# Kernel optimization log

Hardware: AMD Instinct MI355X
Metric: run time of the kernel (lower is better)

The kernel has to match this reference:

```python
import jax, jax.numpy as jnp
import numpy as np

D_MODEL = 512
BINS = 64


def setup_inputs() -> dict:
    key = jax.random.key(0)
    ks = jax.random.split(key, 5)
    x = jax.random.normal(ks[0], (1, 512, D_MODEL), dtype=jnp.float32)
    # torch Linear(2d, d): weight [d, 2d]; store transposed [2d, d] for x @ W
    s1 = 1.0 / np.sqrt(2 * D_MODEL)
    W1 = jax.random.uniform(ks[1], (2 * D_MODEL, D_MODEL), jnp.float32, -s1, s1)
    b1 = jax.random.uniform(ks[2], (D_MODEL,), jnp.float32, -s1, s1)
    s2 = 1.0 / np.sqrt(D_MODEL)
    W2 = jax.random.uniform(ks[3], (D_MODEL, BINS), jnp.float32, -s2, s2)
    b2 = jax.random.uniform(ks[4], (BINS,), jnp.float32, -s2, s2)
    return {"x": x, "W1": W1, "b1": b1, "W2": W2, "b2": b2}


def reference(x, W1, b1, W2, b2):
    # pair = cat([xi, xj], -1); Linear(cat) == xi @ W1[:d] + xj @ W1[d:]
    # This factorization is exact and avoids materializing the [B,N,N,2d] tensor.
    d = x.shape[-1]
    hi = jnp.einsum('bnd,de->bne', x, W1[:d])      # [B, N, d]
    hj = jnp.einsum('bnd,de->bne', x, W1[d:])      # [B, N, d]
    h = hi[:, :, None, :] + hj[:, None, :, :] + b1  # [B, N, N, d]
    h = jax.nn.gelu(h, approximate=False)           # torch nn.GELU default is exact
    return jnp.einsum('bijd,de->bije', h, W2) + b2  # [B, N, N, bins]
```

## Files before the change

kernel.cpp:

```cpp
#include <hip/hip_runtime.h>
#include <hip/hip_fp16.h>

#define D 512
#define NTOK 512
#define BINS 64

typedef float v4f __attribute__((ext_vector_type(4)));
typedef int v4i __attribute__((ext_vector_type(4)));
typedef short short8 __attribute__((ext_vector_type(8)));
typedef _Float16 h8 __attribute__((ext_vector_type(8)));
typedef _Float16 h4 __attribute__((ext_vector_type(4)));

__device__ __forceinline__ __half2 gelu2(__half2 x) {
    __half2 s = __hmul2(x, x);
    __half2 q = __hmul2(x, __hfma2(s, __float2half2_rn(-0.1029437f),
                                      __float2half2_rn(-2.3022082f)));
    __half2 e = h2exp2(q);
    __half2 r = h2rcp(__hadd2(e, __float2half2_rn(1.0f)));
    return __hmul2(x, r);
}

__device__ __forceinline__ __half2 bc_h2(int v) { return __builtin_bit_cast(__half2, v); }
__device__ __forceinline__ int bc_i(__half2 v) { return __builtin_bit_cast(int, v); }

__device__ __forceinline__ v4i pack8(v4f a, v4f b) {
    h8 o;
    o[0] = (_Float16)a.x; o[1] = (_Float16)a.y; o[2] = (_Float16)a.z; o[3] = (_Float16)a.w;
    o[4] = (_Float16)b.x; o[5] = (_Float16)b.y; o[6] = (_Float16)b.z; o[7] = (_Float16)b.w;
    return __builtin_bit_cast(v4i, o);
}

__global__ __launch_bounds__(256) void k_pack(const float* __restrict__ x,
                                              const float* __restrict__ W1,
                                              const float* __restrict__ W2,
                                              v4i* __restrict__ Ap,
                                              v4i* __restrict__ Wp,
                                              short8* __restrict__ Bp) {
    const int b = blockIdx.x;
    const int t = threadIdx.x;
    if (b < 32) {
        const int rb = b;
#pragma unroll
        for (int u = 0; u < 4; ++u) {
            const int e = t + 256 * u;
            const int l = e & 63, ks = e >> 6;
            const float* src = x + (size_t)(rb * 16 + (l & 15)) * D + ks * 32 + (l >> 4) * 8;
            v4f a = *(const v4f*)src;
            v4f c = *(const v4f*)(src + 4);
            Ap[(size_t)(rb * 16 + ks) * 64 + l] = pack8(a, c);
        }
    } else if (b < 96) {
        const int nb = b - 32;
#pragma unroll
        for (int u = 0; u < 4; ++u) {
            const int e = t + 256 * u;
            const int l = e & 63, ks = e >> 6;
            const int ng = nb * 16 + (l & 15);
            const float* src = W1 + (size_t)((ng >> 9) * D + ks * 32 + (l >> 4) * 8) * D
                                  + (ng & 511);
            h8 o;
#pragma unroll
            for (int j = 0; j < 8; ++j) o[j] = (_Float16)src[(size_t)j * D];
            Wp[(size_t)(nb * 16 + ks) * 64 + l] = __builtin_bit_cast(v4i, o);
        }
    } else {
        const int tid = (b - 96) * 256 + t;
        const int ll = tid & 63;
        const int nt = (tid >> 6) & 3;
        const int kt = tid >> 8;
        const int colp = nt * 16 + (ll & 15);
        const int krow = kt * 32 + (ll >> 4) * 8;
        short8 v;
#pragma unroll
        for (int u = 0; u < 8; ++u) {
            _Float16 hv = (_Float16)W2[(size_t)(krow + u) * BINS + colp];
            v[u] = __builtin_bit_cast(short, hv);
        }
        Bp[tid] = v;
    }
}

__global__ __launch_bounds__(256) void k_gemm(const v4i* __restrict__ Ap,
                                              const v4i* __restrict__ Wp,
                                              const float* __restrict__ b1,
                                              _Float16* __restrict__ hi,
                                              _Float16* __restrict__ hj) {
    const int l = threadIdx.x & 63;
    const int w = threadIdx.x >> 6;
    const int c = l & 15;
    const int q = l >> 4;
    const int mb = blockIdx.x >> 4;
    const int cb = blockIdx.x & 15;
    const int nb = cb * 4 + w;

    const v4i* ap0 = Ap + (size_t)(mb * 2 + 0) * 16 * 64 + l;
    const v4i* ap1 = Ap + (size_t)(mb * 2 + 1) * 16 * 64 + l;
    const v4i* wp  = Wp + (size_t)nb * 16 * 64 + l;

    v4f acc0 = {0.f, 0.f, 0.f, 0.f};
    v4f acc1 = {0.f, 0.f, 0.f, 0.f};
#pragma unroll 4
    for (int ks = 0; ks < 16; ++ks) {
        v4i a0 = ap0[ks * 64];
        v4i a1 = ap1[ks * 64];
        v4i bb = wp[ks * 64];
        h8 bf = __builtin_bit_cast(h8, bb);
        acc0 = __builtin_amdgcn_mfma_f32_16x16x32_f16(__builtin_bit_cast(h8, a0), bf, acc0, 0, 0, 0);
        acc1 = __builtin_amdgcn_mfma_f32_16x16x32_f16(__builtin_bit_cast(h8, a1), bf, acc1, 0, 0, 0);
    }

    const int ng = nb * 16 + c;
    const float b1v = (ng < D) ? b1[ng] : 0.0f;
    _Float16* dst = (ng < D ? hi : hj) + (ng & 511);
#pragma unroll
    for (int mf = 0; mf < 2; ++mf) {
        v4f acc = mf ? acc1 : acc0;
        const int row0 = mb * 32 + mf * 16 + q * 4;
#pragma unroll
        for (int r = 0; r < 4; ++r)
            dst[(size_t)(row0 + r) * D] = (_Float16)(acc[r] + b1v);
    }
}

__global__ __launch_bounds__(256) void k_main(const __half* __restrict__ hi,
                                              const __half* __restrict__ hj,
                                              const v4i* __restrict__ Bp,
                                              const float* __restrict__ b2,
                                              float* __restrict__ out) {
    const int l = threadIdx.x & 63;
    const int w = threadIdx.x >> 6;
    const int c = l & 15;
    const int q = l >> 4;
    const int ib = (blockIdx.x >> 5) * 16;
    const int j0 = (blockIdx.x & 31) * 16;

    __shared__ __align__(16) short hic[16][72];
    __shared__ __align__(16) short hjc[16][72];

    const int t = threadIdx.x;
    const int lr = (t & 127) >> 3;
    const int lc = (t & 7) * 8;
    const __half* gsrc = (t < 128 ? hi + (size_t)(ib + lr) * D
                                  : hj + (size_t)(j0 + lr) * D) + lc;
    short* ldst = (t < 128 ? &hic[lr][lc] : &hjc[lr][lc]);

    v4f acc[4][4] = {};
    v4i pf = *(const v4i*)gsrc;

    for (int chunk = 0; chunk < 8; ++chunk) {
        *(v4i*)ldst = pf;
        __syncthreads();
        if (chunk < 7) pf = *(const v4i*)(gsrc + (chunk + 1) * 64);
        const int kt4 = chunk * 8;
#pragma unroll
        for (int h = 0; h < 2; ++h) {
            const int ko = h * 32 + q * 8;
            v4i hjraw = *(const v4i*)&hjc[c][ko];
            __half2 j0h = bc_h2(hjraw.x), j1h = bc_h2(hjraw.y);
            __half2 j2h = bc_h2(hjraw.z), j3h = bc_h2(hjraw.w);
            v4i bfr[4];
#pragma unroll
            for (int nt = 0; nt < 4; ++nt)
                bfr[nt] = Bp[(kt4 + h * 4 + nt) * 64 + l];
#pragma unroll
            for (int p = 0; p < 4; ++p) {
                v4i ar = *(const v4i*)&hic[w * 4 + p][ko];
                __half2 g0 = gelu2(__hadd2(bc_h2(ar.x), j0h));
                __half2 g1 = gelu2(__hadd2(bc_h2(ar.y), j1h));
                __half2 g2 = gelu2(__hadd2(bc_h2(ar.z), j2h));
                __half2 g3 = gelu2(__hadd2(bc_h2(ar.w), j3h));
                v4i ai = {bc_i(g0), bc_i(g1), bc_i(g2), bc_i(g3)};
                h8 af = __builtin_bit_cast(h8, ai);
#pragma unroll
                for (int nt = 0; nt < 4; ++nt)
                    acc[p][nt] = __builtin_amdgcn_mfma_f32_16x16x32_f16(
                        af, __builtin_bit_cast(h8, bfr[nt]), acc[p][nt], 0, 0, 0);
            }
        }
        __syncthreads();
    }

    const int i0 = ib + w * 4;
#pragma unroll
    for (int p = 0; p < 4; ++p) {
        const size_t rowbase = ((size_t)(i0 + p) * NTOK + j0 + q * 4) * BINS;
#pragma unroll
        for (int nt = 0; nt < 4; ++nt) {
            const float bb = b2[nt * 16 + c];
            float* op = out + rowbase + nt * 16 + c;
#pragma unroll
            for (int rr = 0; rr < 4; ++rr)
                op[(size_t)rr * BINS] = acc[p][nt][rr] + bb;
        }
    }
}

extern "C" void kernel_launch(void* const* d_in, const int* in_sizes, int n_in,
                              void* d_out, int out_size, void* d_ws, size_t ws_size,
                              hipStream_t stream) {
    const float* x  = (const float*)d_in[0];
    const float* W1 = (const float*)d_in[1];
    const float* b1 = (const float*)d_in[2];
    const float* W2 = (const float*)d_in[3];
    const float* b2 = (const float*)d_in[4];
    float* out = (float*)d_out;

    char* ws = (char*)d_ws;
    __half* hi = (__half*)ws;
    __half* hj = (__half*)(ws + (512u << 10));
    short8* Bp = (short8*)(ws + (1u << 20));
    v4i*    Ap = (v4i*)(ws + (1u << 20) + (64u << 10));
    v4i*    Wp = (v4i*)(ws + (1u << 20) + (64u << 10) + (512u << 10));

    k_pack<<<112, 256, 0, stream>>>(x, W1, W2, Ap, Wp, Bp);
    k_gemm<<<256, 256, 0, stream>>>(Ap, Wp, b1, (_Float16*)hi, (_Float16*)hj);
    k_main<<<1024, 256, 0, stream>>>(hi, hj, (const v4i*)Bp, b2, out);
}
```

Baseline: 129.1 us.

## Spread pack and GEMM over more blocks, drop LDS staging in main kernel

The W1 pack now uses one thread per packed element across 256 blocks instead of four per thread over 64 blocks. The hi/hj GEMM computes one 16-row tile per block over 512 blocks, giving more parallelism at the cost of reloading the W tiles twice as often. The main kernel no longer stages hi/hj in shared memory with barriers. Each wave reads its operands straight from global or L2, and launch_bounds(256,4) is set to favour occupancy. This removes the syncthreads and LDS traffic but adds redundant global loads across waves.

```diff
diff --git a/kernel.cpp b/kernel.cpp
--- a/kernel.cpp
+++ b/kernel.cpp
@@ -49,22 +49,20 @@
             v4f c = *(const v4f*)(src + 4);
             Ap[(size_t)(rb * 16 + ks) * 64 + l] = pack8(a, c);
         }
-    } else if (b < 96) {
-        const int nb = b - 32;
+    } else if (b < 288) {
+        const int slot = (b - 32) * 256 + t;
+        const int l = slot & 63;
+        const int ks = (slot >> 6) & 15;
+        const int nb = slot >> 10;
+        const int ng = nb * 16 + (l & 15);
+        const float* src = W1 + (size_t)((ng >> 9) * D + ks * 32 + (l >> 4) * 8) * D
+                              + (ng & 511);
+        h8 o;
 #pragma unroll
-        for (int u = 0; u < 4; ++u) {
-            const int e = t + 256 * u;
-            const int l = e & 63, ks = e >> 6;
-            const int ng = nb * 16 + (l & 15);
-            const float* src = W1 + (size_t)((ng >> 9) * D + ks * 32 + (l >> 4) * 8) * D
-                                  + (ng & 511);
-            h8 o;
-#pragma unroll
-            for (int j = 0; j < 8; ++j) o[j] = (_Float16)src[(size_t)j * D];
-            Wp[(size_t)(nb * 16 + ks) * 64 + l] = __builtin_bit_cast(v4i, o);
-        }
+        for (int j = 0; j < 8; ++j) o[j] = (_Float16)src[(size_t)j * D];
+        Wp[(size_t)(nb * 16 + ks) * 64 + l] = __builtin_bit_cast(v4i, o);
     } else {
-        const int tid = (b - 96) * 256 + t;
+        const int tid = (b - 288) * 256 + t;
         const int ll = tid & 63;
         const int nt = (tid >> 6) & 3;
         const int kt = tid >> 8;
@@ -93,40 +91,32 @@
     const int cb = blockIdx.x & 15;
     const int nb = cb * 4 + w;
 
-    const v4i* ap0 = Ap + (size_t)(mb * 2 + 0) * 16 * 64 + l;
-    const v4i* ap1 = Ap + (size_t)(mb * 2 + 1) * 16 * 64 + l;
-    const v4i* wp  = Wp + (size_t)nb * 16 * 64 + l;
+    const v4i* ap = Ap + (size_t)mb * 16 * 64 + l;
+    const v4i* wp = Wp + (size_t)nb * 16 * 64 + l;
 
-    v4f acc0 = {0.f, 0.f, 0.f, 0.f};
-    v4f acc1 = {0.f, 0.f, 0.f, 0.f};
+    v4f acc = {0.f, 0.f, 0.f, 0.f};
 #pragma unroll 4
     for (int ks = 0; ks < 16; ++ks) {
-        v4i a0 = ap0[ks * 64];
-        v4i a1 = ap1[ks * 64];
+        v4i a0 = ap[ks * 64];
         v4i bb = wp[ks * 64];
-        h8 bf = __builtin_bit_cast(h8, bb);
-        acc0 = __builtin_amdgcn_mfma_f32_16x16x32_f16(__builtin_bit_cast(h8, a0), bf, acc0, 0, 0, 0);
-        acc1 = __builtin_amdgcn_mfma_f32_16x16x32_f16(__builtin_bit_cast(h8, a1), bf, acc1, 0, 0, 0);
+        acc = __builtin_amdgcn_mfma_f32_16x16x32_f16(__builtin_bit_cast(h8, a0),
+                                                     __builtin_bit_cast(h8, bb), acc, 0, 0, 0);
     }
 
     const int ng = nb * 16 + c;
     const float b1v = (ng < D) ? b1[ng] : 0.0f;
     _Float16* dst = (ng < D ? hi : hj) + (ng & 511);
+    const int row0 = mb * 16 + q * 4;
 #pragma unroll
-    for (int mf = 0; mf < 2; ++mf) {
-        v4f acc = mf ? acc1 : acc0;
-        const int row0 = mb * 32 + mf * 16 + q * 4;
-#pragma unroll
-        for (int r = 0; r < 4; ++r)
-            dst[(size_t)(row0 + r) * D] = (_Float16)(acc[r] + b1v);
-    }
+    for (int r = 0; r < 4; ++r)
+        dst[(size_t)(row0 + r) * D] = (_Float16)(acc[r] + b1v);
 }
 
-__global__ __launch_bounds__(256) void k_main(const __half* __restrict__ hi,
-                                              const __half* __restrict__ hj,
-                                              const v4i* __restrict__ Bp,
-                                              const float* __restrict__ b2,
-                                              float* __restrict__ out) {
+__global__ __launch_bounds__(256, 4) void k_main(const __half* __restrict__ hi,
+                                                 const __half* __restrict__ hj,
+                                                 const v4i* __restrict__ Bp,
+                                                 const float* __restrict__ b2,
+                                                 float* __restrict__ out) {
     const int l = threadIdx.x & 63;
     const int w = threadIdx.x >> 6;
     const int c = l & 15;
@@ -134,50 +124,35 @@
     const int ib = (blockIdx.x >> 5) * 16;
     const int j0 = (blockIdx.x & 31) * 16;
 
-    __shared__ __align__(16) short hic[16][72];
-    __shared__ __align__(16) short hjc[16][72];
-
-    const int t = threadIdx.x;
-    const int lr = (t & 127) >> 3;
-    const int lc = (t & 7) * 8;
-    const __half* gsrc = (t < 128 ? hi + (size_t)(ib + lr) * D
-                                  : hj + (size_t)(j0 + lr) * D) + lc;
-    short* ldst = (t < 128 ? &hic[lr][lc] : &hjc[lr][lc]);
+    const __half* hjp = hj + (size_t)(j0 + c) * D + q * 8;
+    const __half* hip = hi + (size_t)(ib + w * 4) * D + q * 8;
+    const v4i* bp = Bp + l;
 
     v4f acc[4][4] = {};
-    v4i pf = *(const v4i*)gsrc;
 
-    for (int chunk = 0; chunk < 8; ++chunk) {
-        *(v4i*)ldst = pf;
-        __syncthreads();
-        if (chunk < 7) pf = *(const v4i*)(gsrc + (chunk + 1) * 64);
-        const int kt4 = chunk * 8;
+    for (int kt = 0; kt < 16; ++kt) {
+        const int ko = kt * 32;
+        v4i hjraw = *(const v4i*)(hjp + ko);
+        __half2 j0h = bc_h2(hjraw.x), j1h = bc_h2(hjraw.y);
+        __half2 j2h = bc_h2(hjraw.z), j3h = bc_h2(hjraw.w);
+        v4i bfr[4];
 #pragma unroll
-        for (int h = 0; h < 2; ++h) {
-            const int ko = h * 32 + q * 8;
-            v4i hjraw = *(const v4i*)&hjc[c][ko];
-            __half2 j0h = bc_h2(hjraw.x), j1h = bc_h2(hjraw.y);
-            __half2 j2h = bc_h2(hjraw.z), j3h = bc_h2(hjraw.w);
-            v4i bfr[4];
+        for (int nt = 0; nt < 4; ++nt)
+            bfr[nt] = bp[(kt * 4 + nt) * 64];
+#pragma unroll
+        for (int p = 0; p < 4; ++p) {
+            v4i ar = *(const v4i*)(hip + (size_t)p * D + ko);
+            __half2 g0 = gelu2(__hadd2(bc_h2(ar.x), j0h));
+            __half2 g1 = gelu2(__hadd2(bc_h2(ar.y), j1h));
+            __half2 g2 = gelu2(__hadd2(bc_h2(ar.z), j2h));
+            __half2 g3 = gelu2(__hadd2(bc_h2(ar.w), j3h));
+            v4i ai = {bc_i(g0), bc_i(g1), bc_i(g2), bc_i(g3)};
+            h8 af = __builtin_bit_cast(h8, ai);
 #pragma unroll
             for (int nt = 0; nt < 4; ++nt)
-                bfr[nt] = Bp[(kt4 + h * 4 + nt) * 64 + l];
-#pragma unroll
-            for (int p = 0; p < 4; ++p) {
-                v4i ar = *(const v4i*)&hic[w * 4 + p][ko];
-                __half2 g0 = gelu2(__hadd2(bc_h2(ar.x), j0h));
-                __half2 g1 = gelu2(__hadd2(bc_h2(ar.y), j1h));
-                __half2 g2 = gelu2(__hadd2(bc_h2(ar.z), j2h));
-                __half2 g3 = gelu2(__hadd2(bc_h2(ar.w), j3h));
-                v4i ai = {bc_i(g0), bc_i(g1), bc_i(g2), bc_i(g3)};
-                h8 af = __builtin_bit_cast(h8, ai);
-#pragma unroll
-                for (int nt = 0; nt < 4; ++nt)
-                    acc[p][nt] = __builtin_amdgcn_mfma_f32_16x16x32_f16(
-                        af, __builtin_bit_cast(h8, bfr[nt]), acc[p][nt], 0, 0, 0);
-            }
+                acc[p][nt] = __builtin_amdgcn_mfma_f32_16x16x32_f16(
+                    af, __builtin_bit_cast(h8, bfr[nt]), acc[p][nt], 0, 0, 0);
         }
-        __syncthreads();
     }
 
     const int i0 = ib + w * 4;
@@ -212,7 +187,7 @@
     v4i*    Ap = (v4i*)(ws + (1u << 20) + (64u << 10));
     v4i*    Wp = (v4i*)(ws + (1u << 20) + (64u << 10) + (512u << 10));
 
-    k_pack<<<112, 256, 0, stream>>>(x, W1, W2, Ap, Wp, Bp);
-    k_gemm<<<256, 256, 0, stream>>>(Ap, Wp, b1, (_Float16*)hi, (_Float16*)hj);
+    k_pack<<<304, 256, 0, stream>>>(x, W1, W2, Ap, Wp, Bp);
+    k_gemm<<<512, 256, 0, stream>>>(Ap, Wp, b1, (_Float16*)hi, (_Float16*)hj);
     k_main<<<1024, 256, 0, stream>>>(hi, hj, (const v4i*)Bp, b2, out);
 }
```

After: 127.4 us. Within noise of the previous version (-1.3%).
